# Performance work log

Hardware: AMD Instinct MI355X
Metric: run time of the kernel (lower is better)

## Reference

```python
import jax, jax.numpy as jnp
import numpy as np

B, H, W, C = 8, 64, 64, 768
NH, HD = 12, 64          # num_heads, head_dim
WS = 16                  # window size
SCALE = HD ** -0.5


def setup_inputs() -> dict:
    key = jax.random.key(0)
    ks = jax.random.split(key, 6)
    x = jax.random.normal(ks[0], (B, H * W, C), dtype=jnp.float32)
    w_qkv = jax.random.normal(ks[1], (3 * C, C), dtype=jnp.float32) * 0.02
    w_out = jax.random.normal(ks[2], (C, C), dtype=jnp.float32) * 0.02
    b_out = jnp.zeros((C,), dtype=jnp.float32)
    rel_pos_h = jax.random.normal(ks[3], (2 * WS - 1, HD), dtype=jnp.float32) * 0.02
    rel_pos_w = jax.random.normal(ks[4], (2 * WS - 1, HD), dtype=jnp.float32) * 0.02
    return {"x": x, "w_qkv": w_qkv, "w_out": w_out, "b_out": b_out,
            "rel_pos_h": rel_pos_h, "rel_pos_w": rel_pos_w}


def reference(x, w_qkv, w_out, b_out, rel_pos_h, rel_pos_w):
    nh_w, nw_w = H // WS, W // WS
    xw = x.reshape(B, nh_w, WS, nw_w, WS, C).transpose(0, 1, 3, 2, 4, 5)
    Bw = B * nh_w * nw_w
    t = WS * WS
    xw = xw.reshape(Bw, t, C)

    # ---- qkv projection (no bias) and rearrange 'b t (qkv l d) -> qkv b l t d'
    qkv = (xw @ w_qkv.T).reshape(Bw, t, 3, NH, HD).transpose(2, 0, 3, 1, 4)
    q, k, v = qkv[0], qkv[1], qkv[2]        # each (Bw, NH, t, HD)

    # ---- scaled attention scores
    att = jnp.einsum('bhxd,bhyd->bhxy', q, k) * SCALE   # (Bw, NH, t, t)

    # ---- decomposed relative position bias (SAM/MViT style, q_size == k_size == WS)
    idx = jnp.arange(WS)[:, None] - jnp.arange(WS)[None, :] + (WS - 1)  # (WS, WS)
    Rh = rel_pos_h[idx]                      # (WS, WS, HD)
    Rw = rel_pos_w[idx]                      # (WS, WS, HD)
    rq = q.reshape(Bw * NH, WS, WS, HD)
    rel_h = jnp.einsum('bhwc,hkc->bhwk', rq, Rh)   # (Bw*NH, WS, WS, WS)
    rel_w = jnp.einsum('bhwc,wkc->bhwk', rq, Rw)
    att = (att.reshape(Bw * NH, WS, WS, WS, WS)
           + rel_h[:, :, :, :, None]
           + rel_w[:, :, :, None, :]).reshape(Bw, NH, t, t)

    # ---- softmax + AV
    att = jax.nn.softmax(att, axis=-1)
    o = jnp.einsum('bhxy,bhyd->bhxd', att, v)          # (Bw, NH, t, HD)
    o = o.transpose(0, 2, 1, 3).reshape(Bw, t, C)      # 'b h l d -> b l (h d)'

    # ---- output projection
    o = o @ w_out.T + b_out

    # ---- window unpartition back to (B, H*W, C)
    o = o.reshape(B, nh_w, nw_w, WS, WS, C).transpose(0, 1, 3, 2, 4, 5)
    return o.reshape(B, H * W, C)
```

## Files before the change

### kernel.cpp

```cpp
#include <hip/hip_runtime.h>

typedef __attribute__((ext_vector_type(8))) short bf16x8;
typedef __attribute__((ext_vector_type(4))) float f32x4;
typedef unsigned short u16;

__device__ __forceinline__ u16 f2bf(float f) {
  union { float f; unsigned u; } v; v.f = f;
  unsigned r = v.u + 0x7fffu + ((v.u >> 16) & 1u);
  return (u16)(r >> 16);
}
__device__ __forceinline__ float bf2f(u16 u) {
  union { unsigned u; float f; } v; v.u = ((unsigned)u) << 16;
  return v.f;
}
__device__ __forceinline__ void gload16(const void* g, void* l) {
  __builtin_amdgcn_global_load_lds((const __attribute__((address_space(1))) void*)g,
                                   (__attribute__((address_space(3))) void*)l, 16, 0, 0);
}

#define PH_BAR __builtin_amdgcn_s_barrier()
#define LGKM0  asm volatile("s_waitcnt lgkmcnt(0)" ::: "memory")
#define VM6    asm volatile("s_waitcnt vmcnt(6)" ::: "memory")

__global__ void sab_cvt_kernel(const float* __restrict__ src, u16* __restrict__ dst, int n4) {
  int i = blockIdx.x * blockDim.x + threadIdx.x;
  if (i >= n4) return;
  float4 f = reinterpret_cast<const float4*>(src)[i];
  ushort4 o; o.x = f2bf(f.x); o.y = f2bf(f.y); o.z = f2bf(f.z); o.w = f2bf(f.w);
  reinterpret_cast<ushort4*>(dst)[i] = o;
}

__global__ void sab_xw_kernel(const float* __restrict__ x, u16* __restrict__ xw) {
  const int r = blockIdx.x;
  const int w = r >> 8, tt = r & 255;
  const int b = w >> 4, h1 = (w >> 2) & 3, w1 = w & 3;
  const int i = tt >> 4, j = tt & 15;
  const long xrow = (long)b * 4096 + (h1 * 16 + i) * 64 + w1 * 16 + j;
  const float4* src = reinterpret_cast<const float4*>(x + xrow * 768);
  ushort4* dst = reinterpret_cast<ushort4*>(xw + (long)r * 768);
  const int c = threadIdx.x;
  float4 f = src[c];
  ushort4 o; o.x = f2bf(f.x); o.y = f2bf(f.y); o.z = f2bf(f.z); o.w = f2bf(f.w);
  dst[c] = o;
}

template<int EPI>
__global__ __launch_bounds__(512, 2)
void sab_gemm8_kernel(const u16* __restrict__ A, const u16* __restrict__ Bt,
                      u16* __restrict__ outB, u16* __restrict__ vTp,
                      float* __restrict__ outF, const float* __restrict__ bias,
                      const int K)
{
  __shared__ __align__(16) u16 lds[2][2][2][8192];
  const int tid = threadIdx.x;
  const int lane = tid & 63, wid = tid >> 6;
  const int wr = wid >> 2, wc = wid & 3;
  const int lr = lane & 15, lg = lane >> 4;

  const int nwg = gridDim.x * gridDim.y;
  const int bid0 = blockIdx.y * gridDim.x + blockIdx.x;
  const int bid = (bid0 & 7) * (nwg >> 3) + (bid0 >> 3);
  const long m0 = (long)(bid % gridDim.x) * 256;
  const long n0 = (long)(bid / gridDim.x) * 256;

  const int swz = ((lane & 7) ^ (lane >> 3)) << 3;
  const u16* Agl = A  + (m0 + wid * 8 + (lane >> 3)) * (long)K + swz;
  const u16* Bgl = Bt + (n0 + wid * 8 + (lane >> 3)) * (long)K + swz;

  f32x4 acc[8][4];
#pragma unroll
  for (int a = 0; a < 8; ++a)
#pragma unroll
    for (int b = 0; b < 4; ++b) acc[a][b] = (f32x4){0.f, 0.f, 0.f, 0.f};

  auto stage = [&](int buf, int mat, int half, int rb, int kt) {
    const u16* g = (mat ? Bgl : Agl) + (half * 128 + rb) * (long)K + kt;
    gload16(g, &lds[buf][mat][half][(rb + wid * 8) * 64]);
  };
  auto rdA4 = [&](int buf, int q, bf16x8 (&out)[4][2]) {
#pragma unroll
    for (int m2 = 0; m2 < 4; ++m2)
#pragma unroll
      for (int kc = 0; kc < 2; ++kc)
        out[m2][kc] = *reinterpret_cast<const bf16x8*>(
          &lds[buf][0][wr][(q * 64 + m2 * 16 + lr) * 64 + ((kc * 32 + lg * 8) ^ ((lr & 7) << 3))]);
  };
  auto rdB2 = [&](int buf, int q, bf16x8 (&out)[2][2]) {
#pragma unroll
    for (int n2 = 0; n2 < 2; ++n2)
#pragma unroll
      for (int kc = 0; kc < 2; ++kc)
        out[n2][kc] = *reinterpret_cast<const bf16x8*>(
          &lds[buf][1][wc >> 1][((wc & 1) * 64 + q * 32 + n2 * 16 + lr) * 64 + ((kc * 32 + lg * 8) ^ ((lr & 7) << 3))]);
  };
  auto mma16 = [&](bf16x8 (&a)[4][2], bf16x8 (&b)[2][2], int mq, int nq) {
    __builtin_amdgcn_s_setprio(1);
#pragma unroll
    for (int kc = 0; kc < 2; ++kc)
#pragma unroll
      for (int m2 = 0; m2 < 4; ++m2)
#pragma unroll
        for (int n2 = 0; n2 < 2; ++n2)
          acc[mq * 4 + m2][nq * 2 + n2] = __builtin_amdgcn_mfma_f32_16x16x32_bf16(
              a[m2][kc], b[n2][kc], acc[mq * 4 + m2][nq * 2 + n2], 0, 0, 0);
    __builtin_amdgcn_s_setprio(0);
  };

  stage(0,0,0,0,0);  stage(0,0,1,0,0);  stage(0,1,0,0,0);  stage(0,1,1,0,0);
  stage(0,1,0,64,0); stage(0,1,1,64,0); stage(0,0,0,64,0); stage(0,0,1,64,0);
  stage(1,0,0,0,64); stage(1,0,1,0,64); stage(1,1,0,0,64); stage(1,1,1,0,64);
  stage(1,1,0,64,64); stage(1,1,1,64,64);
  VM6; PH_BAR;

  bf16x8 af[4][2], b0[2][2], b1[2][2];

  for (int kt = 0; kt < K; kt += 128) {
    const int k2 = kt + 128, k3 = kt + 192;
    const bool s2 = k2 < K, s3 = k3 < K;
    rdA4(0, 0, af); rdB2(0, 0, b0);
    stage(1,0,0,64, kt + 64); stage(1,0,1,64, kt + 64);
    PH_BAR; LGKM0; mma16(af, b0, 0, 0); PH_BAR;
    rdB2(0, 1, b1);
    if (s2) { stage(0,0,0,0, k2); stage(0,0,1,0, k2); }
    PH_BAR; LGKM0; mma16(af, b1, 0, 1); PH_BAR;
    rdA4(0, 1, af);
    if (s2) { stage(0,1,0,0, k2); stage(0,1,1,0, k2); }
    PH_BAR; LGKM0; mma16(af, b0, 1, 0); PH_BAR;
    if (s2) { stage(0,1,0,64, k2); stage(0,1,1,64, k2); }
    PH_BAR; mma16(af, b1, 1, 1); VM6; PH_BAR;
    rdA4(1, 0, af); rdB2(1, 0, b0);
    if (s2) { stage(0,0,0,64, k2); stage(0,0,1,64, k2); }
    PH_BAR; LGKM0; mma16(af, b0, 0, 0); PH_BAR;
    rdB2(1, 1, b1);
    if (s3) { stage(1,0,0,0, k3); stage(1,0,1,0, k3); }
    PH_BAR; LGKM0; mma16(af, b1, 0, 1); PH_BAR;
    rdA4(1, 1, af);
    if (s3) { stage(1,1,0,0, k3); stage(1,1,1,0, k3); }
    PH_BAR; LGKM0; mma16(af, b0, 1, 0); PH_BAR;
    if (s3) { stage(1,1,0,64, k3); stage(1,1,1,64, k3); }
    PH_BAR; mma16(af, b1, 1, 1); VM6; PH_BAR;
  }

#pragma unroll
  for (int mt = 0; mt < 8; ++mt)
#pragma unroll
    for (int nt = 0; nt < 4; ++nt) {
      const long col = n0 + wc * 64 + nt * 16 + lr;
      const long row0 = m0 + wr * 128 + mt * 16 + lg * 4;
      if (EPI == 0) {
        if (n0 < 1536) {
#pragma unroll
          for (int r = 0; r < 4; ++r)
            outB[(row0 + r) * 1536 + col] = f2bf(acc[mt][nt][r]);
        } else {
          ushort4 o;
          o.x = f2bf(acc[mt][nt][0]); o.y = f2bf(acc[mt][nt][1]);
          o.z = f2bf(acc[mt][nt][2]); o.w = f2bf(acc[mt][nt][3]);
          *reinterpret_cast<ushort4*>(&vTp[(col - 1536) * 32768L + row0]) = o;
        }
      } else {
        const float bv = bias[col];
#pragma unroll
        for (int r = 0; r < 4; ++r) {
          const int rr = (int)(row0 + r);
          const int w = rr >> 8, tt = rr & 255;
          const long xrow = (long)(w >> 4) * 4096 + (((w >> 2) & 3) * 16 + (tt >> 4)) * 64 + (w & 3) * 16 + (tt & 15);
          outF[xrow * 768 + col] = acc[mt][nt][r] + bv;
        }
      }
    }
}

__global__ __launch_bounds__(256, 2)
void sab_attn_kernel(const u16* __restrict__ qk, const u16* __restrict__ vT,
                     const float* __restrict__ rph, const float* __restrict__ rpw,
                     u16* __restrict__ oatt)
{
  __shared__ __align__(16) u16 relh_s[256 * 16];
  __shared__ __align__(16) u16 relw_s[256 * 16];
  __shared__ __align__(16) u16 Sbuf[4][64 * 72];

  const int blk0 = blockIdx.x;
  const int blk = (blk0 & 7) * 192 + (blk0 >> 3);
  const int w = blk / 12, h = blk % 12;
  const long qbase = (long)w * 256;
  const int tid = threadIdx.x, lane = tid & 63, wid = tid >> 6;
  const int lr = lane & 15, lg = lane >> 4;

  const u16* Qp = qk + (long)h * 64;
  const u16* Kp = qk + 768 + (long)h * 64;
  const u16* Vt = vT + (long)h * 64 * 32768 + w * 256;

#pragma unroll
  for (int ii = 0; ii < 4; ++ii) {
    const int i = wid * 4 + ii;
    f32x4 acc = (f32x4){0.f, 0.f, 0.f, 0.f};
#pragma unroll
    for (int kc = 0; kc < 2; ++kc) {
      bf16x8 a = *reinterpret_cast<const bf16x8*>(&Qp[(qbase + i * 16 + lr) * 1536 + kc * 32 + lg * 8]);
      const float* bp = rph + (i - lr + 15) * 64 + kc * 32 + lg * 8;
      bf16x8 b;
#pragma unroll
      for (int e = 0; e < 8; ++e) b[e] = (short)f2bf(bp[e]);
      acc = __builtin_amdgcn_mfma_f32_16x16x32_bf16(a, b, acc, 0, 0, 0);
    }
#pragma unroll
    for (int r = 0; r < 4; ++r)
      relh_s[(i * 16 + lg * 4 + r) * 16 + lr] = f2bf(acc[r]);
  }
#pragma unroll
  for (int jj = 0; jj < 4; ++jj) {
    const int j = wid * 4 + jj;
    f32x4 acc = (f32x4){0.f, 0.f, 0.f, 0.f};
#pragma unroll
    for (int kc = 0; kc < 2; ++kc) {
      bf16x8 a = *reinterpret_cast<const bf16x8*>(&Qp[(qbase + lr * 16 + j) * 1536 + kc * 32 + lg * 8]);
      const float* bp = rpw + (j - lr + 15) * 64 + kc * 32 + lg * 8;
      bf16x8 b;
#pragma unroll
      for (int e = 0; e < 8; ++e) b[e] = (short)f2bf(bp[e]);
      acc = __builtin_amdgcn_mfma_f32_16x16x32_bf16(a, b, acc, 0, 0, 0);
    }
#pragma unroll
    for (int r = 0; r < 4; ++r)
      relw_s[((lg * 4 + r) * 16 + j) * 16 + lr] = f2bf(acc[r]);
  }
  __syncthreads();

  bf16x8 qa[4][2];
#pragma unroll
  for (int mt = 0; mt < 4; ++mt)
#pragma unroll
    for (int kc = 0; kc < 2; ++kc)
      qa[mt][kc] = *reinterpret_cast<const bf16x8*>(&Qp[(qbase + wid * 64 + mt * 16 + lr) * 1536 + kc * 32 + lg * 8]);

  float rw[4][4];
#pragma unroll
  for (int mt = 0; mt < 4; ++mt)
#pragma unroll
    for (int r = 0; r < 4; ++r)
      rw[mt][r] = bf2f(relw_s[(wid * 64 + mt * 16 + lg * 4 + r) * 16 + lr]);

  float mrun[4][4], lrun[4][4];
  f32x4 oacc[4][4];
#pragma unroll
  for (int mt = 0; mt < 4; ++mt)
#pragma unroll
    for (int r = 0; r < 4; ++r) { mrun[mt][r] = -1e30f; lrun[mt][r] = 0.f; }
#pragma unroll
  for (int mt = 0; mt < 4; ++mt)
#pragma unroll
    for (int nt = 0; nt < 4; ++nt) oacc[mt][nt] = (f32x4){0.f, 0.f, 0.f, 0.f};

  u16* sb = &Sbuf[wid][0];

  for (int kb = 0; kb < 4; ++kb) {
    bf16x8 kf[4][2], vf[4][2];
#pragma unroll
    for (int nt = 0; nt < 4; ++nt)
#pragma unroll
      for (int kc = 0; kc < 2; ++kc) {
        kf[nt][kc] = *reinterpret_cast<const bf16x8*>(&Kp[(qbase + kb * 64 + nt * 16 + lr) * 1536 + kc * 32 + lg * 8]);
        vf[nt][kc] = *reinterpret_cast<const bf16x8*>(&Vt[(nt * 16 + lr) * 32768L + kb * 64 + kc * 32 + lg * 8]);
      }

#pragma unroll
    for (int mt = 0; mt < 4; ++mt) {
      f32x4 sn[4];
#pragma unroll
      for (int nt = 0; nt < 4; ++nt) {
        f32x4 t = (f32x4){0.f, 0.f, 0.f, 0.f};
#pragma unroll
        for (int kc = 0; kc < 2; ++kc)
          t = __builtin_amdgcn_mfma_f32_16x16x32_bf16(qa[mt][kc], kf[nt][kc], t, 0, 0, 0);
        sn[nt] = t;
      }
#pragma unroll
      for (int r = 0; r < 4; ++r) {
        const int x = wid * 64 + mt * 16 + lg * 4 + r;
        float sv[4];
#pragma unroll
        for (int nt = 0; nt < 4; ++nt)
          sv[nt] = sn[nt][r] * 0.125f + bf2f(relh_s[x * 16 + kb * 4 + nt]) + rw[mt][r];
        float rmax = fmaxf(fmaxf(sv[0], sv[1]), fmaxf(sv[2], sv[3]));
        rmax = fmaxf(rmax, __shfl_xor(rmax, 1));
        rmax = fmaxf(rmax, __shfl_xor(rmax, 2));
        rmax = fmaxf(rmax, __shfl_xor(rmax, 4));
        rmax = fmaxf(rmax, __shfl_xor(rmax, 8));
        const float mnew = fmaxf(mrun[mt][r], rmax);
        const float sf = __expf(mrun[mt][r] - mnew);
        mrun[mt][r] = mnew;
        float rsum = 0.f;
#pragma unroll
        for (int nt = 0; nt < 4; ++nt) { const float p = __expf(sv[nt] - mnew); sv[nt] = p; rsum += p; }
        rsum += __shfl_xor(rsum, 1);
        rsum += __shfl_xor(rsum, 2);
        rsum += __shfl_xor(rsum, 4);
        rsum += __shfl_xor(rsum, 8);
        lrun[mt][r] = lrun[mt][r] * sf + rsum;
#pragma unroll
        for (int nt = 0; nt < 4; ++nt) oacc[mt][nt][r] *= sf;
        const int rowl = mt * 16 + lg * 4 + r;
#pragma unroll
        for (int nt = 0; nt < 4; ++nt) sb[rowl * 72 + nt * 16 + lr] = f2bf(sv[nt]);
      }
    }

#pragma unroll
    for (int kc = 0; kc < 2; ++kc)
#pragma unroll
      for (int mt = 0; mt < 4; ++mt) {
        bf16x8 pa = *reinterpret_cast<const bf16x8*>(&sb[(mt * 16 + lr) * 72 + kc * 32 + lg * 8]);
#pragma unroll
        for (int nt = 0; nt < 4; ++nt)
          oacc[mt][nt] = __builtin_amdgcn_mfma_f32_16x16x32_bf16(pa, vf[nt][kc], oacc[mt][nt], 0, 0, 0);
      }
  }

#pragma unroll
  for (int mt = 0; mt < 4; ++mt)
#pragma unroll
    for (int r = 0; r < 4; ++r) {
      const float inv = 1.f / lrun[mt][r];
      const long row = qbase + wid * 64 + mt * 16 + lg * 4 + r;
#pragma unroll
      for (int nt = 0; nt < 4; ++nt)
        oatt[row * 768 + h * 64 + nt * 16 + lr] = f2bf(oacc[mt][nt][r] * inv);
    }
}

extern "C" void kernel_launch(void* const* d_in, const int* in_sizes, int n_in,
                              void* d_out, int out_size, void* d_ws, size_t ws_size,
                              hipStream_t stream) {
  (void)in_sizes; (void)n_in; (void)out_size; (void)ws_size;
  const float* x     = (const float*)d_in[0];
  const float* w_qkv = (const float*)d_in[1];
  const float* w_out = (const float*)d_in[2];
  const float* b_out = (const float*)d_in[3];
  const float* rph   = (const float*)d_in[4];
  const float* rpw   = (const float*)d_in[5];
  float* out = (float*)d_out;

  char* ws = (char*)d_ws;
  u16* qk    = (u16*)ws;
  u16* vT    = (u16*)(ws + 100663296L);
  u16* xw    = (u16*)(ws + 150994944L);
  u16* wqkvb = (u16*)(ws + 201326592L);
  u16* woutb = (u16*)(ws + 204865536L);
  u16* oatt  = xw;

  sab_cvt_kernel<<<dim3(1728), dim3(256), 0, stream>>>(w_qkv, wqkvb, 442368);
  sab_cvt_kernel<<<dim3(576), dim3(256), 0, stream>>>(w_out, woutb, 147456);
  sab_xw_kernel<<<dim3(32768), dim3(192), 0, stream>>>(x, xw);
  sab_gemm8_kernel<0><<<dim3(128, 9), dim3(512), 0, stream>>>(xw, wqkvb, qk, vT, nullptr, nullptr, 768);
  sab_attn_kernel<<<dim3(1536), dim3(256), 0, stream>>>(qk, vT, rph, rpw, oatt);
  sab_gemm8_kernel<1><<<dim3(128, 3), dim3(512), 0, stream>>>(oatt, woutb, nullptr, nullptr, out, b_out, 768);
}
```

Before: 371.7 us.

## Stage GEMM epilogue through LDS, remap tiles per XCD, prefetch first K/V block

The QKV GEMM epilogue now writes bf16 results into LDS first and then stores coalesced 16-byte chunks to global memory, for both the row-major QK output and the transposed V output. This replaces scattered 2-byte stores. The tile-to-XCD mapping changes so each XCD owns a contiguous set of M tiles and walks across N. In the attention kernel the first K/V block loads are hoisted above the relative-position computation, the kb loop is unrolled, and launch bounds rise to 3 blocks per CU, which may increase register pressure or cause spills.

Result: slower. 528.6 us (+42.2%).

```diff
diff --git a/kernel.cpp b/kernel.cpp
--- a/kernel.cpp
+++ b/kernel.cpp
@@ -21,6 +21,7 @@
 #define PH_BAR __builtin_amdgcn_s_barrier()
 #define LGKM0  asm volatile("s_waitcnt lgkmcnt(0)" ::: "memory")
 #define VM6    asm volatile("s_waitcnt vmcnt(6)" ::: "memory")
+#define VM0    asm volatile("s_waitcnt vmcnt(0)" ::: "memory")
 
 __global__ void sab_cvt_kernel(const float* __restrict__ src, u16* __restrict__ dst, int n4) {
   int i = blockIdx.x * blockDim.x + threadIdx.x;
@@ -57,11 +58,11 @@
   const int wr = wid >> 2, wc = wid & 3;
   const int lr = lane & 15, lg = lane >> 4;
 
-  const int nwg = gridDim.x * gridDim.y;
+  const int NY = gridDim.y;
   const int bid0 = blockIdx.y * gridDim.x + blockIdx.x;
-  const int bid = (bid0 & 7) * (nwg >> 3) + (bid0 >> 3);
-  const long m0 = (long)(bid % gridDim.x) * 256;
-  const long n0 = (long)(bid / gridDim.x) * 256;
+  const int xcd = bid0 & 7, local = bid0 >> 3;
+  const long m0 = (long)(xcd * 16 + local / NY) * 256;
+  const long n0 = (long)(local % NY) * 256;
 
   const int swz = ((lane & 7) ^ (lane >> 3)) << 3;
   const u16* Agl = A  + (m0 + wid * 8 + (lane >> 3)) * (long)K + swz;
@@ -141,25 +142,59 @@
     PH_BAR; mma16(af, b1, 1, 1); VM6; PH_BAR;
   }
 
-#pragma unroll
-  for (int mt = 0; mt < 8; ++mt)
-#pragma unroll
-    for (int nt = 0; nt < 4; ++nt) {
-      const long col = n0 + wc * 64 + nt * 16 + lr;
-      const long row0 = m0 + wr * 128 + mt * 16 + lg * 4;
-      if (EPI == 0) {
-        if (n0 < 1536) {
+  VM0;
+  __syncthreads();
+  u16* cl = &lds[0][0][0][0];
+
+  if (EPI == 0) {
+    if (n0 < 1536) {
+#pragma unroll
+      for (int mt = 0; mt < 8; ++mt)
+#pragma unroll
+        for (int nt = 0; nt < 4; ++nt) {
+          const int col = wc * 64 + nt * 16 + lr;
+          const int row0 = wr * 128 + mt * 16 + lg * 4;
 #pragma unroll
           for (int r = 0; r < 4; ++r)
-            outB[(row0 + r) * 1536 + col] = f2bf(acc[mt][nt][r]);
-        } else {
+            cl[(row0 + r) * 256 + col] = f2bf(acc[mt][nt][r]);
+        }
+      __syncthreads();
+#pragma unroll
+      for (int s = 0; s < 16; ++s) {
+        const int c = s * 512 + tid;
+        const int row = c >> 5, ch = c & 31;
+        *reinterpret_cast<bf16x8*>(&outB[(m0 + row) * 1536 + n0 + ch * 8]) =
+            *reinterpret_cast<const bf16x8*>(&cl[row * 256 + ch * 8]);
+      }
+    } else {
+#pragma unroll
+      for (int mt = 0; mt < 8; ++mt)
+#pragma unroll
+        for (int nt = 0; nt < 4; ++nt) {
+          const int col = wc * 64 + nt * 16 + lr;
+          const int row0 = wr * 128 + mt * 16 + lg * 4;
           ushort4 o;
           o.x = f2bf(acc[mt][nt][0]); o.y = f2bf(acc[mt][nt][1]);
           o.z = f2bf(acc[mt][nt][2]); o.w = f2bf(acc[mt][nt][3]);
-          *reinterpret_cast<ushort4*>(&vTp[(col - 1536) * 32768L + row0]) = o;
+          *reinterpret_cast<ushort4*>(&cl[col * 256 + row0]) = o;
         }
-      } else {
+      __syncthreads();
+#pragma unroll
+      for (int s = 0; s < 16; ++s) {
+        const int c = s * 512 + tid;
+        const int d = c >> 5, ch = c & 31;
+        *reinterpret_cast<bf16x8*>(&vTp[(n0 - 1536 + d) * 32768L + m0 + ch * 8]) =
+            *reinterpret_cast<const bf16x8*>(&cl[d * 256 + ch * 8]);
+      }
+    }
+  } else {
+#pragma unroll
+    for (int mt = 0; mt < 8; ++mt)
+#pragma unroll
+      for (int nt = 0; nt < 4; ++nt) {
+        const long col = n0 + wc * 64 + nt * 16 + lr;
         const float bv = bias[col];
+        const long row0 = m0 + wr * 128 + mt * 16 + lg * 4;
 #pragma unroll
         for (int r = 0; r < 4; ++r) {
           const int rr = (int)(row0 + r);
@@ -168,10 +203,10 @@
           outF[xrow * 768 + col] = acc[mt][nt][r] + bv;
         }
       }
-    }
-}
-
-__global__ __launch_bounds__(256, 2)
+  }
+}
+
+__global__ __launch_bounds__(256, 3)
 void sab_attn_kernel(const u16* __restrict__ qk, const u16* __restrict__ vT,
                      const float* __restrict__ rph, const float* __restrict__ rpw,
                      u16* __restrict__ oatt)
@@ -191,6 +226,19 @@
   const u16* Kp = qk + 768 + (long)h * 64;
   const u16* Vt = vT + (long)h * 64 * 32768 + w * 256;
 
+  bf16x8 kf[4][2], vf[4][2];
+#pragma unroll
+  for (int nt = 0; nt < 4; ++nt)
+#pragma unroll
+    for (int kc = 0; kc < 2; ++kc) {
+      kf[nt][kc] = *reinterpret_cast<const bf16x8*>(&Kp[(qbase + nt * 16 + lr) * 1536 + kc * 32 + lg * 8]);
+      vf[nt][kc] = *reinterpret_cast<const bf16x8*>(&Vt[(nt * 16 + lr) * 32768L + kc * 32 + lg * 8]);
+    }
+#pragma unroll
+  for (int nt = 0; nt < 4; ++nt) {
+    asm volatile("" :: "v"(vf[nt][0]), "v"(vf[nt][1]));
+  }
+
 #pragma unroll
   for (int ii = 0; ii < 4; ++ii) {
     const int i = wid * 4 + ii;
@@ -254,15 +302,21 @@
 
   u16* sb = &Sbuf[wid][0];
 
+#pragma unroll
   for (int kb = 0; kb < 4; ++kb) {
-    bf16x8 kf[4][2], vf[4][2];
-#pragma unroll
-    for (int nt = 0; nt < 4; ++nt)
-#pragma unroll
-      for (int kc = 0; kc < 2; ++kc) {
-        kf[nt][kc] = *reinterpret_cast<const bf16x8*>(&Kp[(qbase + kb * 64 + nt * 16 + lr) * 1536 + kc * 32 + lg * 8]);
-        vf[nt][kc] = *reinterpret_cast<const bf16x8*>(&Vt[(nt * 16 + lr) * 32768L + kb * 64 + kc * 32 + lg * 8]);
-      }
+    if (kb > 0) {
+#pragma unroll
+      for (int nt = 0; nt < 4; ++nt)
+#pragma unroll
+        for (int kc = 0; kc < 2; ++kc) {
+          kf[nt][kc] = *reinterpret_cast<const bf16x8*>(&Kp[(qbase + kb * 64 + nt * 16 + lr) * 1536 + kc * 32 + lg * 8]);
+          vf[nt][kc] = *reinterpret_cast<const bf16x8*>(&Vt[(nt * 16 + lr) * 32768L + kb * 64 + kc * 32 + lg * 8]);
+        }
+#pragma unroll
+      for (int nt = 0; nt < 4; ++nt) {
+        asm volatile("" :: "v"(vf[nt][0]), "v"(vf[nt][1]));
+      }
+    }
 
 #pragma unroll
     for (int mt = 0; mt < 4; ++mt) {
```
